# Optimization experiments

Hardware: AMD Instinct MI355X
Metric: run time of the kernel (lower is better)

Reference implementation:

```python
import jax, jax.numpy as jnp
import numpy as np

D_MODEL = 512
N_HEADS = 8
HEAD_DIM = D_MODEL // N_HEADS
BATCH = 2
SEQ = 4096
MAX_SEQ = 4096


def _rope_tables(max_len, dim):
    # freqs = 1/10000^(arange(0,dim,2)/dim); outer(t, freqs); polar -> cos/sin
    inv = 1.0 / (10000.0 ** (np.arange(0, dim, 2, dtype=np.float32) / dim))
    t = np.arange(max_len, dtype=np.float32)
    ang = np.outer(t, inv)  # [max_len, dim/2]
    return jnp.asarray(np.cos(ang)), jnp.asarray(np.sin(ang))


def _apply_rope(x, cos, sin):
    # x: [B, S, H, Hd]; complex-pair rotation over last dim pairs
    B, S, H, Hd = x.shape
    xr = x.reshape(B, S, H, Hd // 2, 2)
    xe, xo = xr[..., 0], xr[..., 1]
    c = cos[:S][None, :, None, :]  # [1,S,1,Hd/2]
    s = sin[:S][None, :, None, :]
    re = xe * c - xo * s
    im = xe * s + xo * c
    return jnp.stack([re, im], axis=-1).reshape(B, S, H, Hd)


def setup_inputs() -> dict:
    key = jax.random.key(0)
    kx, kq, kk, kv, ko = jax.random.split(key, 5)
    std = 1.0 / np.sqrt(D_MODEL)
    return {
        "x": jax.random.normal(kx, (BATCH, SEQ, D_MODEL), dtype=jnp.float32),
        "Wq": jax.random.normal(kq, (D_MODEL, D_MODEL), dtype=jnp.float32) * std,
        "Wk": jax.random.normal(kk, (D_MODEL, D_MODEL), dtype=jnp.float32) * std,
        "Wv": jax.random.normal(kv, (D_MODEL, D_MODEL), dtype=jnp.float32) * std,
        "Wo": jax.random.normal(ko, (D_MODEL, D_MODEL), dtype=jnp.float32) * std,
    }


def reference(x, Wq, Wk, Wv, Wo):
    B, S, D = x.shape
    cos, sin = _rope_tables(MAX_SEQ, HEAD_DIM)
    # nn.Linear: y = x @ W.T
    q = (x @ Wq.T).reshape(B, S, N_HEADS, HEAD_DIM)
    k = (x @ Wk.T).reshape(B, S, N_HEADS, HEAD_DIM)
    v = (x @ Wv.T).reshape(B, S, N_HEADS, HEAD_DIM)
    q = _apply_rope(q, cos, sin)
    k = _apply_rope(k, cos, sin)
    scale = HEAD_DIM ** (-0.5)
    # [B,H,S,S]
    scores = jnp.einsum("bshd,bthd->bhst", q, k) * scale
    causal = jnp.tril(jnp.ones((S, S), dtype=bool))
    scores = jnp.where(causal[None, None], scores, -jnp.inf)
    attn = jax.nn.softmax(scores, axis=-1)
    out = jnp.einsum("bhst,bthd->bshd", attn, v).reshape(B, S, D)
    return out @ Wo.T
```

## Files before the change

### kernel.cpp

```cpp
#include <hip/hip_runtime.h>
#include <hip/hip_bf16.h>
#include <math.h>

#define D_MODEL 512
#define N_HEADS 8
#define HEAD_DIM 64
#define BATCH 2
#define SEQ 4096
#define M_ROWS (BATCH*SEQ)

typedef __attribute__((ext_vector_type(8))) short short8;
typedef __attribute__((ext_vector_type(4))) float f32x4;

__device__ inline short f2bf(float f) {
  union { float f; unsigned u; } v; v.f = f;
  unsigned u = v.u;
  unsigned r = u + 0x7FFFu + ((u >> 16) & 1u);
  return (short)(r >> 16);
}

__device__ inline unsigned cvtpk_bf16(float lo, float hi) {
  unsigned r;
  asm("v_cvt_pk_bf16_f32 %0, %1, %2" : "=v"(r) : "v"(lo), "v"(hi));
  return r;
}

__device__ inline void gll16(const void* g, void* l) {
  __builtin_amdgcn_global_load_lds(
      (const __attribute__((address_space(1))) unsigned int*)g,
      (__attribute__((address_space(3))) unsigned int*)l, 16, 0, 0);
}

__device__ inline short8 cvt8(float4 a, float4 b) {
  short8 o;
  o[0] = f2bf(a.x); o[1] = f2bf(a.y); o[2] = f2bf(a.z); o[3] = f2bf(a.w);
  o[4] = f2bf(b.x); o[5] = f2bf(b.y); o[6] = f2bf(b.z); o[7] = f2bf(b.w);
  return o;
}

#define XOCT (M_ROWS*D_MODEL/8)
#define WOCT (3*D_MODEL*D_MODEL/8)
#define OOCT (D_MODEL*D_MODEL/8)
__global__ void prep_kernel(const float* __restrict__ x,
                            const float* __restrict__ Wq,
                            const float* __restrict__ Wk,
                            const float* __restrict__ Wv,
                            const float* __restrict__ Wo,
                            short* __restrict__ xb,
                            short* __restrict__ Wqkv,
                            short* __restrict__ Wob,
                            float* __restrict__ cosT,
                            float* __restrict__ sinT) {
  int i = blockIdx.x * blockDim.x + threadIdx.x;
  if (i < XOCT) {
    float4 a = *(const float4*)&x[i * 8];
    float4 b = *(const float4*)&x[i * 8 + 4];
    *(short8*)&xb[i * 8] = cvt8(a, b);
  }
  if (i < WOCT) {
    int e = i * 8;
    int t = e >> 18, r = e & 262143;
    const float* W = (t == 0) ? Wq : ((t == 1) ? Wk : Wv);
    float4 a = *(const float4*)&W[r];
    float4 b = *(const float4*)&W[r + 4];
    *(short8*)&Wqkv[e] = cvt8(a, b);
  }
  if (i < OOCT) {
    float4 a = *(const float4*)&Wo[i * 8];
    float4 b = *(const float4*)&Wo[i * 8 + 4];
    *(short8*)&Wob[i * 8] = cvt8(a, b);
  }
  if (i < SEQ * 32) {
    int s = i >> 5, p = i & 31;
    float e = (float)(2 * p) * (1.0f / 64.0f);
    float inv = powf(10000.0f, -e);
    float ang = (float)s * inv;
    float sv, cv;
    sincosf(ang, &sv, &cv);
    cosT[i] = cv; sinT[i] = sv;
  }
}

template<int MODE>
__global__ __launch_bounds__(256) void gemm_kernel(const short* __restrict__ A,
                                                   const short* __restrict__ B,
                                                   float* __restrict__ out_f,
                                                   short* __restrict__ Qb,
                                                   short* __restrict__ Kb,
                                                   short* __restrict__ Vb,
                                                   const float* __restrict__ cosT,
                                                   const float* __restrict__ sinT) {
  __shared__ short smem[18432];
  short (*Cs)[136] = (short(*)[136])smem;

  const int m0 = blockIdx.x * 128;
  const int n0 = blockIdx.y * 128;
  const int tid = threadIdx.x;
  const int lane = tid & 63, wid = tid >> 6;
  const int wm = wid >> 1, wn = wid & 1;
  const int l15 = lane & 15, g = lane >> 4;

  const int srow8 = lane >> 3;
  const int sblk = (lane & 7) ^ srow8;

  f32x4 acc[4][4] = {};

  for (int kt = 0; kt < 512; kt += 64) {
    __syncthreads();
#pragma unroll
    for (int cc = 0; cc < 4; ++cc) {
      int r0 = (cc * 4 + wid) * 8;
      int row = r0 + srow8;
      gll16(&A[(m0 + row) * 512 + kt + sblk * 8], smem + (cc * 4 + wid) * 512);
      gll16(&B[(n0 + row) * 512 + kt + sblk * 8], smem + 8192 + (cc * 4 + wid) * 512);
    }
    __syncthreads();
#pragma unroll
    for (int kk = 0; kk < 64; kk += 32) {
      short8 a[4], b[4];
#pragma unroll
      for (int mi = 0; mi < 4; ++mi) {
        int row = wm * 64 + mi * 16 + l15;
        a[mi] = *(const short8*)&smem[row * 64 + ((((kk >> 3) + g) ^ (l15 & 7)) << 3)];
      }
#pragma unroll
      for (int ni = 0; ni < 4; ++ni) {
        int row = wn * 64 + ni * 16 + l15;
        b[ni] = *(const short8*)&smem[8192 + row * 64 + ((((kk >> 3) + g) ^ (l15 & 7)) << 3)];
      }
#pragma unroll
      for (int mi = 0; mi < 4; ++mi)
#pragma unroll
        for (int ni = 0; ni < 4; ++ni)
          acc[mi][ni] = __builtin_amdgcn_mfma_f32_16x16x32_bf16(a[mi], b[ni], acc[mi][ni], 0, 0, 0);
    }
  }

  if (MODE == 1) {
    for (int mi = 0; mi < 4; ++mi)
      for (int ni = 0; ni < 4; ++ni)
        for (int r = 0; r < 4; ++r) {
          int row_g = m0 + wm * 64 + mi * 16 + (g << 2) + r;
          int col_g = n0 + wn * 64 + ni * 16 + l15;
          out_f[row_g * 512 + col_g] = acc[mi][ni][r];
        }
    return;
  }

  const int t_blk = n0 >> 9;
  __syncthreads();

  if (t_blk < 2) {
    const float qs = (t_blk == 0) ? 0.18033688011112042f : 1.0f;
    for (int mi = 0; mi < 4; ++mi)
      for (int ni = 0; ni < 4; ++ni)
        for (int r = 0; r < 4; ++r) {
          int lrow = wm * 64 + mi * 16 + (g << 2) + r;
          int ss = (m0 + lrow) & 4095;
          int d = (n0 + wn * 64 + ni * 16 + l15) & 63;
          int p = d >> 1;
          float c = cosT[ss * 32 + p], s = sinT[ss * 32 + p];
          float v = acc[mi][ni][r];
          float partner = __shfl_xor(v, 1);
          float res = (l15 & 1) ? (v * c + partner * s) : (v * c - partner * s);
          Cs[lrow][wn * 64 + ni * 16 + l15] = f2bf(res * qs);
        }
  } else {
    for (int mi = 0; mi < 4; ++mi)
      for (int ni = 0; ni < 4; ++ni)
        for (int r = 0; r < 4; ++r)
          Cs[wm * 64 + mi * 16 + (g << 2) + r][wn * 64 + ni * 16 + l15] =
              f2bf(acc[mi][ni][r]);
  }
  __syncthreads();

  if (t_blk < 2) {
    short* dst = (t_blk == 0) ? Qb : Kb;
#pragma unroll
    for (int it = 0; it < 8; ++it) {
      int row = (tid >> 4) + (it << 4);
      int colb = (tid & 15) << 3;
      short8 vv = *(const short8*)&Cs[row][colb];
      int row_g = m0 + row;
      int ss = row_g & 4095, bb = row_g >> 12;
      int cc = (n0 + colb) & 511;
      int h = cc >> 6, d = cc & 63;
      *(short8*)&dst[(((bb << 3) + h) * SEQ + ss) * 64 + d] = vv;
    }
  } else {
#pragma unroll
    for (int it = 0; it < 8; ++it) {
      int c = tid & 127;
      int sb = ((tid >> 7) << 3) + (it << 4);
      short8 o8;
#pragma unroll
      for (int j = 0; j < 8; ++j) o8[j] = Cs[sb + j][c];
      int row_g0 = m0 + sb;
      int ss = row_g0 & 4095, bb = row_g0 >> 12;
      int cc = (n0 + c) & 511;
      int h = cc >> 6, d = cc & 63;
      *(short8*)&Vb[((long)(((bb << 3) + h) * 64 + d)) * SEQ + ss] = o8;
    }
  }
}

__global__ __launch_bounds__(512, 4) void attn_kernel(const short* __restrict__ Q,
                                                      const short* __restrict__ K,
                                                      const short* __restrict__ Vt,
                                                      short* __restrict__ O) {
  __shared__ short Ks[2][64 * 64];
  __shared__ short Vs[2][64 * 64];

  const int o = blockIdx.x;
  const int j = o >> 4;
  const int bh = o & 15;
  const int tile = (o < 256) ? (31 - j) : (j - 16);

  const int tid = threadIdx.x, lane = tid & 63, w = tid >> 6;
  const int l15 = lane & 15, g = lane >> 4;
  const long base = (long)bh * SEQ * 64;
  const long baseV = (long)bh * 64 * SEQ;
  const int bb = bh >> 3, h = bh & 7;

  const int srow = tid >> 3;
  const int sc16k = (tid & 7) ^ (srow & 7);
  short* ldsSegK0 = &Ks[0][(tid >> 6) << 9];
  short* ldsSegK1 = &Ks[1][(tid >> 6) << 9];
  short* ldsSegV0 = &Vs[0][(tid >> 6) << 9];
  short* ldsSegV1 = &Vs[1][(tid >> 6) << 9];

  const int q0 = (tile << 7) + (w << 4);
  const int nc = 2 * tile + 2;

  short8 aq0 = *(const short8*)&Q[base + (long)(q0 + l15) * 64 + (g << 3)];
  short8 aq1 = *(const short8*)&Q[base + (long)(q0 + l15) * 64 + 32 + (g << 3)];

  f32x4 o_acc[4] = {};
  float m_r = -__builtin_inff(), l_r = 0.f;

  gll16(&K[base + (long)srow * 64 + sc16k * 8], ldsSegK0);
  gll16(&Vt[baseV + (long)srow * SEQ + sc16k * 8], ldsSegV0);

  for (int c = 0; c < nc; ++c) {
    const int kv0 = c << 6;
    const int bi = c & 1;
    __syncthreads();
    if (c + 1 < nc) {
      const int nkv = (c + 1) << 6;
      short* dK = (bi ? ldsSegK0 : ldsSegK1);
      short* dV = (bi ? ldsSegV0 : ldsSegV1);
      gll16(&K[base + (long)(nkv + srow) * 64 + sc16k * 8], dK);
      gll16(&Vt[baseV + (long)srow * SEQ + nkv + sc16k * 8], dV);
    }
    if (kv0 > q0) continue;

    f32x4 sf[4] = {};
    __builtin_amdgcn_s_setprio(1);
#pragma unroll
    for (int f = 0; f < 4; ++f) {
      int row = f * 16 + l15, sw = row & 7;
      short8 bk0 = *(const short8*)&Ks[bi][row * 64 + ((g) ^ sw) * 8];
      short8 bk1 = *(const short8*)&Ks[bi][row * 64 + ((4 + g) ^ sw) * 8];
      sf[f] = __builtin_amdgcn_mfma_f32_16x16x32_bf16(bk0, aq0, sf[f], 0, 0, 0);
      sf[f] = __builtin_amdgcn_mfma_f32_16x16x32_bf16(bk1, aq1, sf[f], 0, 0, 0);
    }
    __builtin_amdgcn_s_setprio(0);
    if (kv0 == (q0 & ~63)) {
      int qrow = q0 + l15;
#pragma unroll
      for (int f = 0; f < 4; ++f)
#pragma unroll
        for (int r = 0; r < 4; ++r) {
          int kvc = kv0 + f * 16 + (g << 2) + r;
          if (kvc > qrow) sf[f][r] = -__builtin_inff();
        }
    }

    float pmx = sf[0][0];
#pragma unroll
    for (int f = 0; f < 4; ++f)
#pragma unroll
      for (int r = 0; r < 4; ++r) pmx = fmaxf(pmx, sf[f][r]);
    if (!__all(pmx <= m_r + 8.f)) {
      float pm = pmx;
      pm = fmaxf(pm, __shfl_xor(pm, 16));
      pm = fmaxf(pm, __shfl_xor(pm, 32));
      float mn = fmaxf(m_r, pm);
      float alpha = exp2f(m_r - mn);
      m_r = mn;
      l_r *= alpha;
#pragma unroll
      for (int r = 0; r < 4; ++r) {
        float ar = __shfl(alpha, (g << 2) + r);
#pragma unroll
        for (int db = 0; db < 4; ++db) o_acc[db][r] *= ar;
      }
    }

    float pr[4][4];
    float s0 = 0.f;
#pragma unroll
    for (int f = 0; f < 4; ++f)
#pragma unroll
      for (int r = 0; r < 4; ++r) {
        float pv = exp2f(sf[f][r] - m_r);
        pr[f][r] = pv;
        s0 += pv;
      }
    l_r += s0;

    unsigned pk[4][2];
#pragma unroll
    for (int f = 0; f < 4; ++f) {
      pk[f][0] = cvtpk_bf16(pr[f][0], pr[f][1]);
      pk[f][1] = cvtpk_bf16(pr[f][2], pr[f][3]);
    }
    unsigned paw0[4], paw1[4];
    const bool hi = (g & 2) != 0;
#pragma unroll
    for (int w2 = 0; w2 < 4; ++w2) {
      int srcl = l15 + ((2 * (g & 1) + (w2 >> 1)) << 4);
      unsigned c0 = (unsigned)__shfl((int)pk[0][w2 & 1], srcl);
      unsigned c1 = (unsigned)__shfl((int)pk[1][w2 & 1], srcl);
      unsigned c2 = (unsigned)__shfl((int)pk[2][w2 & 1], srcl);
      unsigned c3 = (unsigned)__shfl((int)pk[3][w2 & 1], srcl);
      paw0[w2] = hi ? c1 : c0;
      paw1[w2] = hi ? c3 : c2;
    }
    union { unsigned u[4]; short8 s; } u0, u1;
#pragma unroll
    for (int w2 = 0; w2 < 4; ++w2) { u0.u[w2] = paw0[w2]; u1.u[w2] = paw1[w2]; }
    short8 pa0 = u0.s, pa1 = u1.s;

    __builtin_amdgcn_s_setprio(1);
#pragma unroll
    for (int kk = 0; kk < 2; ++kk) {
      short8 pa = kk ? pa1 : pa0;
#pragma unroll
      for (int db = 0; db < 4; ++db) {
        int row = db * 16 + l15, sw = row & 7;
        short8 bv = *(const short8*)&Vs[bi][row * 64 + ((kk * 4 + g) ^ sw) * 8];
        o_acc[db] = __builtin_amdgcn_mfma_f32_16x16x32_bf16(pa, bv, o_acc[db], 0, 0, 0);
      }
    }
    __builtin_amdgcn_s_setprio(0);
  }

  l_r += __shfl_xor(l_r, 16);
  l_r += __shfl_xor(l_r, 32);
#pragma unroll
  for (int db = 0; db < 4; ++db)
#pragma unroll
    for (int r = 0; r < 4; ++r) {
      float lq = __shfl(l_r, (g << 2) + r);
      int s_g = q0 + (g << 2) + r;
      float v = o_acc[db][r] / lq;
      O[((long)(bb * SEQ + s_g)) * 512 + h * 64 + db * 16 + l15] = f2bf(v);
    }
}

extern "C" void kernel_launch(void* const* d_in, const int* in_sizes, int n_in,
                              void* d_out, int out_size, void* d_ws, size_t ws_size,
                              hipStream_t stream) {
  const float* x  = (const float*)d_in[0];
  const float* Wq = (const float*)d_in[1];
  const float* Wk = (const float*)d_in[2];
  const float* Wv = (const float*)d_in[3];
  const float* Wo = (const float*)d_in[4];

  char* ws = (char*)d_ws;
  size_t off = 0;
  auto alloc = [&](size_t bytes) {
    void* p = ws + off;
    off += (bytes + 255) & ~(size_t)255;
    return p;
  };
  short* xb   = (short*)alloc((size_t)M_ROWS * 512 * 2);
  short* Wqkv = (short*)alloc((size_t)1536 * 512 * 2);
  short* Wob  = (short*)alloc((size_t)512 * 512 * 2);
  float* cosT = (float*)alloc((size_t)SEQ * 32 * 4);
  float* sinT = (float*)alloc((size_t)SEQ * 32 * 4);
  short* Qb   = (short*)alloc((size_t)16 * SEQ * 64 * 2);
  short* Kb   = (short*)alloc((size_t)16 * SEQ * 64 * 2);
  short* Vt   = (short*)alloc((size_t)16 * SEQ * 64 * 2);
  short* Obuf = (short*)alloc((size_t)M_ROWS * 512 * 2);

  prep_kernel<<<2048, 256, 0, stream>>>(x, Wq, Wk, Wv, Wo, xb, Wqkv, Wob, cosT, sinT);
  gemm_kernel<0><<<dim3(64, 12), 256, 0, stream>>>(xb, Wqkv, nullptr, Qb, Kb, Vt, cosT, sinT);
  attn_kernel<<<512, 512, 0, stream>>>(Qb, Kb, Vt, Obuf);
  gemm_kernel<1><<<dim3(64, 4), 256, 0, stream>>>(Obuf, Wob, (float*)d_out, nullptr, nullptr, nullptr, nullptr, nullptr);
}
```

Measured before the change: 206.9 us.

## Rewrite attention with 32x32 MFMA, 32-row warps, and paired causal tiles per block

The attention kernel moves from 16x16x32 to 32x32x16 bf16 MFMA, so each wave handles 32 query rows and a block handles 256 queries. The P-matrix relayout uses permlane32_swap instead of many shuffles. Each block processes two query tiles, one from each end of the sequence (pr and 15-pr), to balance the causal work, and the grid is halved to 256 blocks with launch bounds relaxed to 2 blocks per CU. The intent is more MFMA throughput and less shuffle overhead, at the cost of more registers per thread, fewer resident waves, and serial processing of the two tiles within a block.

```diff
diff --git a/kernel.cpp b/kernel.cpp
--- a/kernel.cpp
+++ b/kernel.cpp
@@ -11,6 +11,8 @@
 
 typedef __attribute__((ext_vector_type(8))) short short8;
 typedef __attribute__((ext_vector_type(4))) float f32x4;
+typedef __attribute__((ext_vector_type(16))) float f32x16;
+typedef __attribute__((ext_vector_type(2))) unsigned uint2v;
 
 __device__ inline short f2bf(float f) {
   union { float f; unsigned u; } v; v.f = f;
@@ -36,6 +38,12 @@
   o[0] = f2bf(a.x); o[1] = f2bf(a.y); o[2] = f2bf(a.z); o[3] = f2bf(a.w);
   o[4] = f2bf(b.x); o[5] = f2bf(b.y); o[6] = f2bf(b.z); o[7] = f2bf(b.w);
   return o;
+}
+
+__device__ inline short8 mk8(unsigned a, unsigned b, unsigned c, unsigned d) {
+  union { unsigned u[4]; short8 s; } x;
+  x.u[0] = a; x.u[1] = b; x.u[2] = c; x.u[3] = d;
+  return x.s;
 }
 
 #define XOCT (M_ROWS*D_MODEL/8)
@@ -109,8 +117,7 @@
     __syncthreads();
 #pragma unroll
     for (int cc = 0; cc < 4; ++cc) {
-      int r0 = (cc * 4 + wid) * 8;
-      int row = r0 + srow8;
+      int row = (cc * 4 + wid) * 8 + srow8;
       gll16(&A[(m0 + row) * 512 + kt + sblk * 8], smem + (cc * 4 + wid) * 512);
       gll16(&B[(n0 + row) * 512 + kt + sblk * 8], smem + 8192 + (cc * 4 + wid) * 512);
     }
@@ -204,7 +211,7 @@
   }
 }
 
-__global__ __launch_bounds__(512, 4) void attn_kernel(const short* __restrict__ Q,
+__global__ __launch_bounds__(512, 2) void attn_kernel(const short* __restrict__ Q,
                                                       const short* __restrict__ K,
                                                       const short* __restrict__ Vt,
                                                       short* __restrict__ O) {
@@ -212,151 +219,136 @@
   __shared__ short Vs[2][64 * 64];
 
   const int o = blockIdx.x;
-  const int j = o >> 4;
   const int bh = o & 15;
-  const int tile = (o < 256) ? (31 - j) : (j - 16);
-
+  const int pr = o >> 4;
   const int tid = threadIdx.x, lane = tid & 63, w = tid >> 6;
-  const int l15 = lane & 15, g = lane >> 4;
+  const int l31 = lane & 31, hl = lane >> 5;
   const long base = (long)bh * SEQ * 64;
   const long baseV = (long)bh * 64 * SEQ;
   const int bb = bh >> 3, h = bh & 7;
 
   const int srow = tid >> 3;
   const int sc16k = (tid & 7) ^ (srow & 7);
-  short* ldsSegK0 = &Ks[0][(tid >> 6) << 9];
-  short* ldsSegK1 = &Ks[1][(tid >> 6) << 9];
-  short* ldsSegV0 = &Vs[0][(tid >> 6) << 9];
-  short* ldsSegV1 = &Vs[1][(tid >> 6) << 9];
-
-  const int q0 = (tile << 7) + (w << 4);
-  const int nc = 2 * tile + 2;
-
-  short8 aq0 = *(const short8*)&Q[base + (long)(q0 + l15) * 64 + (g << 3)];
-  short8 aq1 = *(const short8*)&Q[base + (long)(q0 + l15) * 64 + 32 + (g << 3)];
-
-  f32x4 o_acc[4] = {};
-  float m_r = -__builtin_inff(), l_r = 0.f;
-
-  gll16(&K[base + (long)srow * 64 + sc16k * 8], ldsSegK0);
-  gll16(&Vt[baseV + (long)srow * SEQ + sc16k * 8], ldsSegV0);
-
-  for (int c = 0; c < nc; ++c) {
-    const int kv0 = c << 6;
-    const int bi = c & 1;
+  short* segK0 = &Ks[0][(tid >> 6) << 9];
+  short* segK1 = &Ks[1][(tid >> 6) << 9];
+  short* segV0 = &Vs[0][(tid >> 6) << 9];
+  short* segV1 = &Vs[1][(tid >> 6) << 9];
+
+#pragma unroll
+  for (int ti = 0; ti < 2; ++ti) {
+    const int tile = ti ? (15 - pr) : pr;
+    const int q0w = (tile << 8) + (w << 5);
+    const int nc = (tile + 1) << 2;
+
+    short8 qf[4];
+#pragma unroll
+    for (int kb = 0; kb < 4; ++kb)
+      qf[kb] = *(const short8*)&Q[base + (long)(q0w + l31) * 64 + kb * 16 + hl * 8];
+
+    f32x16 oa0 = {}, oa1 = {};
+    float m_r = -__builtin_inff(), l_r = 0.f;
+
     __syncthreads();
-    if (c + 1 < nc) {
-      const int nkv = (c + 1) << 6;
-      short* dK = (bi ? ldsSegK0 : ldsSegK1);
-      short* dV = (bi ? ldsSegV0 : ldsSegV1);
-      gll16(&K[base + (long)(nkv + srow) * 64 + sc16k * 8], dK);
-      gll16(&Vt[baseV + (long)srow * SEQ + nkv + sc16k * 8], dV);
-    }
-    if (kv0 > q0) continue;
-
-    f32x4 sf[4] = {};
-    __builtin_amdgcn_s_setprio(1);
-#pragma unroll
-    for (int f = 0; f < 4; ++f) {
-      int row = f * 16 + l15, sw = row & 7;
-      short8 bk0 = *(const short8*)&Ks[bi][row * 64 + ((g) ^ sw) * 8];
-      short8 bk1 = *(const short8*)&Ks[bi][row * 64 + ((4 + g) ^ sw) * 8];
-      sf[f] = __builtin_amdgcn_mfma_f32_16x16x32_bf16(bk0, aq0, sf[f], 0, 0, 0);
-      sf[f] = __builtin_amdgcn_mfma_f32_16x16x32_bf16(bk1, aq1, sf[f], 0, 0, 0);
-    }
-    __builtin_amdgcn_s_setprio(0);
-    if (kv0 == (q0 & ~63)) {
-      int qrow = q0 + l15;
-#pragma unroll
-      for (int f = 0; f < 4; ++f)
-#pragma unroll
-        for (int r = 0; r < 4; ++r) {
-          int kvc = kv0 + f * 16 + (g << 2) + r;
-          if (kvc > qrow) sf[f][r] = -__builtin_inff();
+    gll16(&K[base + (long)srow * 64 + sc16k * 8], segK0);
+    gll16(&Vt[baseV + (long)srow * SEQ + sc16k * 8], segV0);
+
+    for (int c = 0; c < nc; ++c) {
+      const int kv0 = c << 6;
+      const int bi = c & 1;
+      __syncthreads();
+      if (c + 1 < nc) {
+        const int nkv = (c + 1) << 6;
+        short* dK = (bi ? segK0 : segK1);
+        short* dV = (bi ? segV0 : segV1);
+        gll16(&K[base + (long)(nkv + srow) * 64 + sc16k * 8], dK);
+        gll16(&Vt[baseV + (long)srow * SEQ + nkv + sc16k * 8], dV);
+      }
+      if (kv0 > q0w + 31) continue;
+
+      f32x16 s0 = {}, s1 = {};
+      __builtin_amdgcn_s_setprio(1);
+#pragma unroll
+      for (int kb = 0; kb < 4; ++kb) {
+        int blk = 2 * kb + hl;
+        short8 a0 = *(const short8*)&Ks[bi][l31 * 64 + ((blk ^ (l31 & 7)) << 3)];
+        short8 a1 = *(const short8*)&Ks[bi][(32 + l31) * 64 + ((blk ^ (l31 & 7)) << 3)];
+        s0 = __builtin_amdgcn_mfma_f32_32x32x16_bf16(a0, qf[kb], s0, 0, 0, 0);
+        s1 = __builtin_amdgcn_mfma_f32_32x32x16_bf16(a1, qf[kb], s1, 0, 0, 0);
+      }
+      __builtin_amdgcn_s_setprio(0);
+
+      if (kv0 + 63 > q0w) {
+        int q = q0w + l31;
+#pragma unroll
+        for (int r = 0; r < 16; ++r) {
+          int kvr = kv0 + (r & 3) + ((r >> 2) << 3) + (hl << 2);
+          if (kvr > q) s0[r] = -__builtin_inff();
+          if (kvr + 32 > q) s1[r] = -__builtin_inff();
         }
-    }
-
-    float pmx = sf[0][0];
-#pragma unroll
-    for (int f = 0; f < 4; ++f)
-#pragma unroll
-      for (int r = 0; r < 4; ++r) pmx = fmaxf(pmx, sf[f][r]);
-    if (!__all(pmx <= m_r + 8.f)) {
-      float pm = pmx;
-      pm = fmaxf(pm, __shfl_xor(pm, 16));
-      pm = fmaxf(pm, __shfl_xor(pm, 32));
-      float mn = fmaxf(m_r, pm);
-      float alpha = exp2f(m_r - mn);
-      m_r = mn;
-      l_r *= alpha;
-#pragma unroll
-      for (int r = 0; r < 4; ++r) {
-        float ar = __shfl(alpha, (g << 2) + r);
-#pragma unroll
-        for (int db = 0; db < 4; ++db) o_acc[db][r] *= ar;
-      }
-    }
-
-    float pr[4][4];
-    float s0 = 0.f;
-#pragma unroll
-    for (int f = 0; f < 4; ++f)
-#pragma unroll
-      for (int r = 0; r < 4; ++r) {
-        float pv = exp2f(sf[f][r] - m_r);
-        pr[f][r] = pv;
-        s0 += pv;
-      }
-    l_r += s0;
-
-    unsigned pk[4][2];
-#pragma unroll
-    for (int f = 0; f < 4; ++f) {
-      pk[f][0] = cvtpk_bf16(pr[f][0], pr[f][1]);
-      pk[f][1] = cvtpk_bf16(pr[f][2], pr[f][3]);
-    }
-    unsigned paw0[4], paw1[4];
-    const bool hi = (g & 2) != 0;
-#pragma unroll
-    for (int w2 = 0; w2 < 4; ++w2) {
-      int srcl = l15 + ((2 * (g & 1) + (w2 >> 1)) << 4);
-      unsigned c0 = (unsigned)__shfl((int)pk[0][w2 & 1], srcl);
-      unsigned c1 = (unsigned)__shfl((int)pk[1][w2 & 1], srcl);
-      unsigned c2 = (unsigned)__shfl((int)pk[2][w2 & 1], srcl);
-      unsigned c3 = (unsigned)__shfl((int)pk[3][w2 & 1], srcl);
-      paw0[w2] = hi ? c1 : c0;
-      paw1[w2] = hi ? c3 : c2;
-    }
-    union { unsigned u[4]; short8 s; } u0, u1;
-#pragma unroll
-    for (int w2 = 0; w2 < 4; ++w2) { u0.u[w2] = paw0[w2]; u1.u[w2] = paw1[w2]; }
-    short8 pa0 = u0.s, pa1 = u1.s;
-
-    __builtin_amdgcn_s_setprio(1);
-#pragma unroll
-    for (int kk = 0; kk < 2; ++kk) {
-      short8 pa = kk ? pa1 : pa0;
-#pragma unroll
-      for (int db = 0; db < 4; ++db) {
-        int row = db * 16 + l15, sw = row & 7;
-        short8 bv = *(const short8*)&Vs[bi][row * 64 + ((kk * 4 + g) ^ sw) * 8];
-        o_acc[db] = __builtin_amdgcn_mfma_f32_16x16x32_bf16(pa, bv, o_acc[db], 0, 0, 0);
-      }
-    }
-    __builtin_amdgcn_s_setprio(0);
-  }
-
-  l_r += __shfl_xor(l_r, 16);
-  l_r += __shfl_xor(l_r, 32);
-#pragma unroll
-  for (int db = 0; db < 4; ++db)
-#pragma unroll
-    for (int r = 0; r < 4; ++r) {
-      float lq = __shfl(l_r, (g << 2) + r);
-      int s_g = q0 + (g << 2) + r;
-      float v = o_acc[db][r] / lq;
-      O[((long)(bb * SEQ + s_g)) * 512 + h * 64 + db * 16 + l15] = f2bf(v);
-    }
+      }
+
+      float pmx = s0[0];
+#pragma unroll
+      for (int r = 1; r < 16; ++r) pmx = fmaxf(pmx, s0[r]);
+#pragma unroll
+      for (int r = 0; r < 16; ++r) pmx = fmaxf(pmx, s1[r]);
+      if (!__all(pmx <= m_r + 8.f)) {
+        float pm = fmaxf(pmx, __shfl_xor(pmx, 32));
+        float mn = fmaxf(m_r, pm);
+        float alpha = exp2f(m_r - mn);
+        m_r = mn;
+        l_r *= alpha;
+#pragma unroll
+        for (int r = 0; r < 16; ++r) {
+          int qq = (r & 3) + ((r >> 2) << 3) + (hl << 2);
+          float ar = __shfl(alpha, qq);
+          oa0[r] *= ar; oa1[r] *= ar;
+        }
+      }
+      float sum = 0.f;
+#pragma unroll
+      for (int r = 0; r < 16; ++r) { s0[r] = exp2f(s0[r] - m_r); sum += s0[r]; }
+#pragma unroll
+      for (int r = 0; r < 16; ++r) { s1[r] = exp2f(s1[r] - m_r); sum += s1[r]; }
+      l_r += sum;
+
+      unsigned pw[16];
+#pragma unroll
+      for (int i = 0; i < 8; ++i) pw[i]     = cvtpk_bf16(s0[2 * i], s0[2 * i + 1]);
+#pragma unroll
+      for (int i = 0; i < 8; ++i) pw[8 + i] = cvtpk_bf16(s1[2 * i], s1[2 * i + 1]);
+#pragma unroll
+      for (int gq = 0; gq < 4; ++gq) {
+        uint2v e0 = __builtin_amdgcn_permlane32_swap(pw[gq * 4 + 0], pw[gq * 4 + 2], false, false);
+        uint2v e1 = __builtin_amdgcn_permlane32_swap(pw[gq * 4 + 1], pw[gq * 4 + 3], false, false);
+        pw[gq * 4 + 0] = e0.x; pw[gq * 4 + 2] = e0.y;
+        pw[gq * 4 + 1] = e1.x; pw[gq * 4 + 3] = e1.y;
+      }
+
+      __builtin_amdgcn_s_setprio(1);
+#pragma unroll
+      for (int kb2 = 0; kb2 < 4; ++kb2) {
+        short8 pa = mk8(pw[kb2 * 4], pw[kb2 * 4 + 1], pw[kb2 * 4 + 2], pw[kb2 * 4 + 3]);
+        int blk = 2 * kb2 + hl;
+        short8 bv0 = *(const short8*)&Vs[bi][l31 * 64 + ((blk ^ (l31 & 7)) << 3)];
+        short8 bv1 = *(const short8*)&Vs[bi][(32 + l31) * 64 + ((blk ^ (l31 & 7)) << 3)];
+        oa0 = __builtin_amdgcn_mfma_f32_32x32x16_bf16(pa, bv0, oa0, 0, 0, 0);
+        oa1 = __builtin_amdgcn_mfma_f32_32x32x16_bf16(pa, bv1, oa1, 0, 0, 0);
+      }
+      __builtin_amdgcn_s_setprio(0);
+    }
+
+    float lf = l_r + __shfl_xor(l_r, 32);
+#pragma unroll
+    for (int r = 0; r < 16; ++r) {
+      int qq = (r & 3) + ((r >> 2) << 3) + (hl << 2);
+      float lq = __shfl(lf, qq);
+      int q = q0w + qq;
+      long rowb = ((long)(bb * SEQ + q)) * 512 + h * 64;
+      O[rowb + l31]      = f2bf(oa0[r] / lq);
+      O[rowb + 32 + l31] = f2bf(oa1[r] / lq);
+    }
+  }
 }
 
 extern "C" void kernel_launch(void* const* d_in, const int* in_sizes, int n_in,
@@ -387,6 +379,6 @@
 
   prep_kernel<<<2048, 256, 0, stream>>>(x, Wq, Wk, Wv, Wo, xb, Wqkv, Wob, cosT, sinT);
   gemm_kernel<0><<<dim3(64, 12), 256, 0, stream>>>(xb, Wqkv, nullptr, Qb, Kb, Vt, cosT, sinT);
-  attn_kernel<<<512, 512, 0, stream>>>(Qb, Kb, Vt, Obuf);
+  attn_kernel<<<256, 512, 0, stream>>>(Qb, Kb, Vt, Obuf);
   gemm_kernel<1><<<dim3(64, 4), 256, 0, stream>>>(Obuf, Wob, (float*)d_out, nullptr, nullptr, nullptr, nullptr, nullptr);
 }
```

After: 247.1 us. 1.19x slower.
